# Kernel optimization log

Measured on AMD Instinct MI355X. Metric: run time of the kernel, lower is better.

## Reference

```python
import jax, jax.numpy as jnp
import numpy as np

M = 1024       # input feature dim
T_EXPERTS = 64 # number of experts
K = 2          # top-k
TOKENS = 65536 # B*N flattened tokens


def setup_inputs() -> dict:
    key = jax.random.key(0)
    ks = jax.random.split(key, 6)
    return {
        "x": jax.random.normal(ks[0], (TOKENS, M), dtype=jnp.float32),
        "noise": jax.random.normal(ks[1], (TOKENS, T_EXPERTS), dtype=jnp.float32),
        "Wg_w": jax.random.normal(ks[2], (T_EXPERTS, M), dtype=jnp.float32) * 0.02,
        "Wg_b": jax.random.normal(ks[3], (T_EXPERTS,), dtype=jnp.float32) * 0.02,
        "Wn_w": jax.random.normal(ks[4], (T_EXPERTS, M), dtype=jnp.float32) * 0.02,
        "Wn_b": jax.random.normal(ks[5], (T_EXPERTS,), dtype=jnp.float32) * 0.02,
    }


def reference(x, noise, Wg_w, Wg_b, Wn_w, Wn_b):
    # logits = Wg(x); noise_scale = softplus(Wnoise(x))
    logits = jnp.einsum("bm,tm->bt", x, Wg_w) + Wg_b          # [tokens, t]
    noise_scale = jax.nn.softplus(jnp.einsum("bm,tm->bt", x, Wn_w) + Wn_b)
    H = logits + noise * noise_scale                           # noisy logits
    topk_vals, topk_idx = jax.lax.top_k(H, K)                  # [tokens, k]
    topk_softmax = jax.nn.softmax(topk_vals, axis=-1)
    # scatter softmax weights into sparse [tokens, t] gate tensor
    rows = jnp.arange(H.shape[0])[:, None]
    gates = jnp.zeros_like(H).at[rows, topk_idx].set(topk_softmax)
    return (gates, H, topk_idx, noise_scale, logits)
```

## Files before the change

kernel.cpp:

```cpp
#include <hip/hip_runtime.h>
#include <math.h>

#define NTOK 65536
#define MDIM 1024
#define NE   64
#define TB   128
#define NKC  32
#define DELTA 5e-4f

typedef float f32x4  __attribute__((ext_vector_type(4)));
typedef float f32x2  __attribute__((ext_vector_type(2)));
typedef short bf16x8 __attribute__((ext_vector_type(8)));
typedef unsigned int u32;

__device__ __forceinline__ unsigned short f32_to_bf16_rne(float f) {
    u32 u = __builtin_bit_cast(u32, f);
    u32 r = u + 0x7FFFu + ((u >> 16) & 1u);
    return (unsigned short)(r >> 16);
}
__device__ __forceinline__ float bf16_to_f32(unsigned short h) {
    u32 u = ((u32)h) << 16;
    return __builtin_bit_cast(float, u);
}
__device__ __forceinline__ void gll16(const void* g, void* l) {
    __builtin_amdgcn_global_load_lds(
        (const __attribute__((address_space(1))) u32*)g,
        (__attribute__((address_space(3))) u32*)l, 16, 0, 0);
}
__device__ __forceinline__ void nt_store4(float* p, f32x4 v) {
    __builtin_nontemporal_store(v, (f32x4*)p);
}

__global__ __launch_bounds__(256) void split_w_kernel(
    const float* __restrict__ Wg_w, const float* __restrict__ Wn_w,
    unsigned short* __restrict__ ws, u32* __restrict__ cnt)
{
    if (blockIdx.x == 0 && threadIdx.x == 0) *cnt = 0;

    const int gid  = blockIdx.x * 256 + threadIdx.x;
    const int kc   = gid >> 10;
    const int rest = gid & 1023;
    const int tm   = rest >> 8;
    const int mat  = (rest >> 7) & 1;
    const int sp   = (rest >> 6) & 1;
    const int lane = rest & 63;
    const int e    = (lane & 15) + 16 * tm;
    const int k0   = kc * 32 + 8 * (lane >> 4);
    const float* W = mat ? Wn_w : Wg_w;

    unsigned short o[8];
#pragma unroll
    for (int i = 0; i < 8; ++i) {
        const float v = W[(size_t)e * MDIM + k0 + i];
        const u32 u  = __builtin_bit_cast(u32, v);
        const unsigned short hb = (unsigned short)(u >> 16);
        o[i] = sp ? f32_to_bf16_rne(v - bf16_to_f32(hb)) : hb;
    }
    uint4 pk;
    pk.x = (u32)o[0] | ((u32)o[1] << 16);
    pk.y = (u32)o[2] | ((u32)o[3] << 16);
    pk.z = (u32)o[4] | ((u32)o[5] << 16);
    pk.w = (u32)o[6] | ((u32)o[7] << 16);
    *reinterpret_cast<uint4*>(&ws[(size_t)gid * 8]) = pk;
}

__global__ __launch_bounds__(512, 4) void gate_mfma_kernel(
    const float* __restrict__ x,
    const float* __restrict__ noise,
    const unsigned short* __restrict__ ws,
    const float* __restrict__ Wg_b,
    const float* __restrict__ Wn_b,
    float* __restrict__ out_gates,
    float* __restrict__ out_H,
    float* __restrict__ out_idx,
    float* __restrict__ out_ns,
    float* __restrict__ out_logits,
    u32* __restrict__ cnt,
    u32* __restrict__ list)
{
    __shared__ unsigned short wbuf[2][8192];

    const int tid   = threadIdx.x;
    const int lane  = tid & 63;
    const int w     = tid >> 6;
    const int c     = lane & 15;
    const int q     = lane >> 4;
    const int tokw  = blockIdx.x * TB + w * 16;
    const int phase = blockIdx.x & (NKC - 1);

    const float* __restrict__ xr = x + (size_t)(tokw + c) * MDIM + 8 * q;

    f32x4 acc[4][2];
#pragma unroll
    for (int tm = 0; tm < 4; ++tm)
#pragma unroll
        for (int m = 0; m < 2; ++m)
            acc[tm][m] = (f32x4){0.f, 0.f, 0.f, 0.f};

    f32x4 xa, xb;

#define STAGE(CI, BUF)                                                          \
    {                                                                           \
        const unsigned short* wc_ = ws + (size_t)(CI) * 8192;                   \
        gll16(wc_ + (size_t)tid * 8,         &wbuf[BUF][(size_t)tid * 8]);      \
        gll16(wc_ + (size_t)(tid + 512) * 8, &wbuf[BUF][(size_t)(tid + 512) * 8]); \
        __builtin_amdgcn_sched_barrier(0);                                      \
        xa = *reinterpret_cast<const f32x4*>(xr + (CI) * 32);                   \
        xb = *reinterpret_cast<const f32x4*>(xr + (CI) * 32 + 4);               \
        __builtin_amdgcn_sched_barrier(0);                                      \
    }

    STAGE(phase, 0)
    asm volatile("s_waitcnt vmcnt(2)" ::: "memory");
    __syncthreads();

    int cur = 0;
    for (int kci = 0; kci < NKC; ++kci) {
        asm volatile("s_waitcnt vmcnt(0)" ::: "memory");

        bf16x8 xhi, xlo;
        {
            const float v[8] = {xa.x, xa.y, xa.z, xa.w, xb.x, xb.y, xb.z, xb.w};
            u32 hp[4], lp[4];
#pragma unroll
            for (int p = 0; p < 4; ++p) {
                const u32 u0 = __builtin_bit_cast(u32, v[2 * p]);
                const u32 u1 = __builtin_bit_cast(u32, v[2 * p + 1]);
                const float h0 = __builtin_bit_cast(float, u0 & 0xFFFF0000u);
                const float h1 = __builtin_bit_cast(float, u1 & 0xFFFF0000u);
                hp[p] = (u0 >> 16) | (u1 & 0xFFFF0000u);
                const u32 l0 = (u32)f32_to_bf16_rne(v[2 * p] - h0);
                const u32 l1 = (u32)f32_to_bf16_rne(v[2 * p + 1] - h1);
                lp[p] = l0 | (l1 << 16);
            }
            const uint4 h4 = {hp[0], hp[1], hp[2], hp[3]};
            const uint4 l4 = {lp[0], lp[1], lp[2], lp[3]};
            xhi = __builtin_bit_cast(bf16x8, h4);
            xlo = __builtin_bit_cast(bf16x8, l4);
        }

        if (kci + 1 < NKC) {
            const int kcn = (kci + 1 + phase) & (NKC - 1);
            STAGE(kcn, cur ^ 1)
        }

#pragma unroll
        for (int tm = 0; tm < 4; ++tm)
#pragma unroll
            for (int mat = 0; mat < 2; ++mat) {
                const int gbase = ((tm * 4 + mat * 2) * 64 + lane) * 8;
                const bf16x8 whi = *reinterpret_cast<const bf16x8*>(&wbuf[cur][gbase]);
                const bf16x8 wlo = *reinterpret_cast<const bf16x8*>(&wbuf[cur][gbase + 512]);
                f32x4 a = acc[tm][mat];
                a = __builtin_amdgcn_mfma_f32_16x16x32_bf16(wlo, xhi, a, 0, 0, 0);
                a = __builtin_amdgcn_mfma_f32_16x16x32_bf16(whi, xlo, a, 0, 0, 0);
                a = __builtin_amdgcn_mfma_f32_16x16x32_bf16(whi, xhi, a, 0, 0, 0);
                acc[tm][mat] = a;
            }

        if (kci + 1 < NKC) {
            asm volatile("s_waitcnt vmcnt(2)" ::: "memory");
            __syncthreads();
        }
        cur ^= 1;
    }
#undef STAGE

    f32x4 bgv[4], bnv[4];
#pragma unroll
    for (int tm = 0; tm < 4; ++tm) {
        bgv[tm] = *reinterpret_cast<const f32x4*>(&Wg_b[16 * tm + 4 * q]);
        bnv[tm] = *reinterpret_cast<const f32x4*>(&Wn_b[16 * tm + 4 * q]);
    }

    const int tok = tokw + c;
    float hv[4][4];

#pragma unroll
    for (int tm = 0; tm < 4; ++tm) {
        const size_t rb = (size_t)tok * NE + 16 * tm + 4 * q;
        const f32x4 nz = __builtin_nontemporal_load(
            reinterpret_cast<const f32x4*>(&noise[rb]));
        f32x4 lg, nsv, hh;
#pragma unroll
        for (int r = 0; r < 4; ++r) {
            lg[r] = acc[tm][0][r] + bgv[tm][r];
            const float nl = acc[tm][1][r] + bnv[tm][r];
            nsv[r] = fmaxf(nl, 0.f) + log1pf(expf(-fabsf(nl)));
            hh[r]  = fmaf(nz[r], nsv[r], lg[r]);
            hv[tm][r] = hh[r];
        }
        nt_store4(&out_logits[rb], lg);
        nt_store4(&out_ns[rb],     nsv);
        nt_store4(&out_H[rb],      hh);
    }

    float v1 = -INFINITY, v2 = -INFINITY, v3 = -INFINITY;
    int   i1 = 0,         i2 = 0;
#pragma unroll
    for (int tm = 0; tm < 4; ++tm)
#pragma unroll
        for (int r = 0; r < 4; ++r) {
            const int ex = 16 * tm + 4 * q + r;
            const float hcur = hv[tm][r];
            if (hcur > v1)      { v3 = v2; v2 = v1; i2 = i1; v1 = hcur; i1 = ex; }
            else if (hcur > v2) { v3 = v2; v2 = hcur; i2 = ex; }
            else if (hcur > v3) { v3 = hcur; }
        }

#pragma unroll
    for (int off = 16; off <= 32; off <<= 1) {
        const float w1 = __shfl_xor(v1, off, 64);
        const int   k1 = __shfl_xor(i1, off, 64);
        const float w2 = __shfl_xor(v2, off, 64);
        const int   k2 = __shfl_xor(i2, off, 64);
        const float w3 = __shfl_xor(v3, off, 64);
        float m3;
        if (v1 >= w1) m3 = (v2 >= w1) ? fmaxf(v3, w1) : fmaxf(v2, w2);
        else          m3 = (w2 >= v1) ? fmaxf(w3, v1) : fmaxf(w2, v2);
        if (w1 > v1 || (w1 == v1 && k1 < i1)) {
            if (v1 > w2 || (v1 == w2 && i1 < k2)) { v2 = v1; i2 = i1; }
            else                                  { v2 = w2; i2 = k2; }
            v1 = w1; i1 = k1;
        } else {
            if (w1 > v2 || (w1 == v2 && k1 < i2)) { v2 = w1; i2 = k1; }
        }
        v3 = m3;
    }

    const float e2v = expf(v2 - v1);
    const float inv = 1.f / (1.f + e2v);
    const float p1  = inv;
    const float p2  = e2v * inv;

#pragma unroll
    for (int tm = 0; tm < 4; ++tm) {
        f32x4 g;
#pragma unroll
        for (int r = 0; r < 4; ++r) {
            const int ex = 16 * tm + 4 * q + r;
            g[r] = (ex == i1) ? p1 : ((ex == i2) ? p2 : 0.f);
        }
        nt_store4(&out_gates[(size_t)tok * NE + 16 * tm + 4 * q], g);
    }
    if (q == 0) {
        f32x2 iv;
        iv.x = (float)i1;
        iv.y = (float)i2;
        __builtin_nontemporal_store(iv,
            reinterpret_cast<f32x2*>(&out_idx[(size_t)tok * 2]));
        if ((v1 - v2 < DELTA) || (v2 - v3 < DELTA)) {
            const u32 slot = atomicAdd(cnt, 1u);
            list[slot] = (u32)tok;
        }
    }
}

__global__ __launch_bounds__(64) void refine_kernel(
    const float* __restrict__ x,
    const float* __restrict__ noise,
    const float* __restrict__ Wg_w, const float* __restrict__ Wg_b,
    const float* __restrict__ Wn_w, const float* __restrict__ Wn_b,
    const u32* __restrict__ cnt, const u32* __restrict__ list,
    float* __restrict__ out_gates, float* __restrict__ out_idx)
{
    const int lane = threadIdx.x;
    const u32 n = *cnt;

    for (u32 it = blockIdx.x; it < n; it += gridDim.x) {
        const int tok = (int)list[it];

        f32x4 xv[4];
#pragma unroll
        for (int i = 0; i < 4; ++i)
            xv[i] = *reinterpret_cast<const f32x4*>(
                &x[(size_t)tok * MDIM + lane * 16 + i * 4]);

        float lgv = 0.f, nlv = 0.f;
        for (int e = 0; e < NE; ++e) {
            float sg = 0.f, sn = 0.f;
#pragma unroll
            for (int i = 0; i < 4; ++i) {
                const f32x4 wg = *reinterpret_cast<const f32x4*>(
                    &Wg_w[(size_t)e * MDIM + lane * 16 + i * 4]);
                const f32x4 wn = *reinterpret_cast<const f32x4*>(
                    &Wn_w[(size_t)e * MDIM + lane * 16 + i * 4]);
#pragma unroll
                for (int j = 0; j < 4; ++j) {
                    sg = fmaf(xv[i][j], wg[j], sg);
                    sn = fmaf(xv[i][j], wn[j], sn);
                }
            }
#pragma unroll
            for (int off = 32; off >= 1; off >>= 1) {
                sg += __shfl_xor(sg, off, 64);
                sn += __shfl_xor(sn, off, 64);
            }
            if (e == lane) { lgv = sg; nlv = sn; }
        }

        lgv += Wg_b[lane];
        nlv += Wn_b[lane];
        const float ns = fmaxf(nlv, 0.f) + log1pf(expf(-fabsf(nlv)));
        const float h  = fmaf(noise[(size_t)tok * NE + lane], ns, lgv);

        float v1 = h; int i1 = lane;
#pragma unroll
        for (int off = 32; off >= 1; off >>= 1) {
            const float ov = __shfl_xor(v1, off, 64);
            const int   oi = __shfl_xor(i1, off, 64);
            if (ov > v1 || (ov == v1 && oi < i1)) { v1 = ov; i1 = oi; }
        }
        float v2 = (lane == i1) ? -INFINITY : h; int i2 = lane;
#pragma unroll
        for (int off = 32; off >= 1; off >>= 1) {
            const float ov = __shfl_xor(v2, off, 64);
            const int   oi = __shfl_xor(i2, off, 64);
            if (ov > v2 || (ov == v2 && oi < i2)) { v2 = ov; i2 = oi; }
        }

        const float e2v = expf(v2 - v1);
        const float inv = 1.f / (1.f + e2v);
        const float p1  = inv;
        const float p2  = e2v * inv;

        out_gates[(size_t)tok * NE + lane] =
            (lane == i1) ? p1 : ((lane == i2) ? p2 : 0.f);
        if (lane == 0) {
            *reinterpret_cast<float2*>(&out_idx[(size_t)tok * 2]) =
                make_float2((float)i1, (float)i2);
        }
    }
}

extern "C" void kernel_launch(void* const* d_in, const int* in_sizes, int n_in,
                              void* d_out, int out_size, void* d_ws, size_t ws_size,
                              hipStream_t stream) {
    const float* x     = (const float*)d_in[0];
    const float* noise = (const float*)d_in[1];
    const float* Wg_w  = (const float*)d_in[2];
    const float* Wg_b  = (const float*)d_in[3];
    const float* Wn_w  = (const float*)d_in[4];
    const float* Wn_b  = (const float*)d_in[5];

    float* out = (float*)d_out;
    float* out_gates  = out;
    float* out_H      = out + (size_t)NTOK * NE;
    float* out_idx    = out + (size_t)2 * NTOK * NE;
    float* out_ns     = out + (size_t)2 * NTOK * NE + (size_t)NTOK * 2;
    float* out_logits = out + (size_t)3 * NTOK * NE + (size_t)NTOK * 2;

    unsigned short* wsplit = (unsigned short*)d_ws;
    u32* cnt  = (u32*)((char*)d_ws + 524288);
    u32* list = (u32*)((char*)d_ws + 524304);

    split_w_kernel<<<dim3(128), dim3(256), 0, stream>>>(Wg_w, Wn_w, wsplit, cnt);
    gate_mfma_kernel<<<dim3(NTOK / TB), dim3(512), 0, stream>>>(
        x, noise, wsplit, Wg_b, Wn_b,
        out_gates, out_H, out_idx, out_ns, out_logits, cnt, list);
    refine_kernel<<<dim3(1024), dim3(64), 0, stream>>>(
        x, noise, Wg_w, Wg_b, Wn_w, Wn_b, cnt, list, out_gates, out_idx);
}
```

Before: 123.9 us.

## Prefetch x two chunks ahead with double-buffered register bursts

Loads of x now arrive in bursts of two K-chunks, held in a double-buffered register set, and are issued about two iterations ahead instead of one. Weight staging into LDS stays one chunk ahead. The loop is fully unrolled and the vmcnt waits are adjusted so the compute never waits on the x burst that is still in flight. The goal is to hide global-memory latency for the streamed x reads, at the cost of more VGPRs, which may lower occupancy.

```diff
diff --git a/kernel.cpp b/kernel.cpp
--- a/kernel.cpp
+++ b/kernel.cpp
@@ -86,7 +86,7 @@
     const int c     = lane & 15;
     const int q     = lane >> 4;
     const int tokw  = blockIdx.x * TB + w * 16;
-    const int phase = blockIdx.x & (NKC - 1);
+    const int phase = (blockIdx.x & 15) * 2;
 
     const float* __restrict__ xr = x + (size_t)(tokw + c) * MDIM + 8 * q;
 
@@ -97,74 +97,100 @@
         for (int m = 0; m < 2; ++m)
             acc[tm][m] = (f32x4){0.f, 0.f, 0.f, 0.f};
 
-    f32x4 xa, xb;
-
-#define STAGE(CI, BUF)                                                          \
+    f32x4 xg[2][2][2];
+
+#define WGLL(CI, BUF)                                                           \
     {                                                                           \
         const unsigned short* wc_ = ws + (size_t)(CI) * 8192;                   \
         gll16(wc_ + (size_t)tid * 8,         &wbuf[BUF][(size_t)tid * 8]);      \
         gll16(wc_ + (size_t)(tid + 512) * 8, &wbuf[BUF][(size_t)(tid + 512) * 8]); \
         __builtin_amdgcn_sched_barrier(0);                                      \
-        xa = *reinterpret_cast<const f32x4*>(xr + (CI) * 32);                   \
-        xb = *reinterpret_cast<const f32x4*>(xr + (CI) * 32 + 4);               \
+    }
+#define XBURST(G, SET)                                                          \
+    {                                                                           \
+        const int c0_ = (phase + 2 * (G)) & (NKC - 1);                          \
+        const int c1_ = c0_ + 1;            \
+        xg[SET][0][0] = *reinterpret_cast<const f32x4*>(xr + c0_ * 32);         \
+        xg[SET][0][1] = *reinterpret_cast<const f32x4*>(xr + c0_ * 32 + 4);     \
+        xg[SET][1][0] = *reinterpret_cast<const f32x4*>(xr + c1_ * 32);         \
+        xg[SET][1][1] = *reinterpret_cast<const f32x4*>(xr + c1_ * 32 + 4);     \
         __builtin_amdgcn_sched_barrier(0);                                      \
     }
 
-    STAGE(phase, 0)
-    asm volatile("s_waitcnt vmcnt(2)" ::: "memory");
+    WGLL(phase, 0)
+    XBURST(0, 0)
+    XBURST(1, 1)
+    asm volatile("s_waitcnt vmcnt(8)" ::: "memory");
     __syncthreads();
 
     int cur = 0;
-    for (int kci = 0; kci < NKC; ++kci) {
-        asm volatile("s_waitcnt vmcnt(0)" ::: "memory");
-
-        bf16x8 xhi, xlo;
-        {
-            const float v[8] = {xa.x, xa.y, xa.z, xa.w, xb.x, xb.y, xb.z, xb.w};
-            u32 hp[4], lp[4];
-#pragma unroll
-            for (int p = 0; p < 4; ++p) {
-                const u32 u0 = __builtin_bit_cast(u32, v[2 * p]);
-                const u32 u1 = __builtin_bit_cast(u32, v[2 * p + 1]);
-                const float h0 = __builtin_bit_cast(float, u0 & 0xFFFF0000u);
-                const float h1 = __builtin_bit_cast(float, u1 & 0xFFFF0000u);
-                hp[p] = (u0 >> 16) | (u1 & 0xFFFF0000u);
-                const u32 l0 = (u32)f32_to_bf16_rne(v[2 * p] - h0);
-                const u32 l1 = (u32)f32_to_bf16_rne(v[2 * p + 1] - h1);
-                lp[p] = l0 | (l1 << 16);
-            }
-            const uint4 h4 = {hp[0], hp[1], hp[2], hp[3]};
-            const uint4 l4 = {lp[0], lp[1], lp[2], lp[3]};
-            xhi = __builtin_bit_cast(bf16x8, h4);
-            xlo = __builtin_bit_cast(bf16x8, l4);
-        }
-
-        if (kci + 1 < NKC) {
-            const int kcn = (kci + 1 + phase) & (NKC - 1);
-            STAGE(kcn, cur ^ 1)
-        }
-
-#pragma unroll
-        for (int tm = 0; tm < 4; ++tm)
-#pragma unroll
-            for (int mat = 0; mat < 2; ++mat) {
-                const int gbase = ((tm * 4 + mat * 2) * 64 + lane) * 8;
-                const bf16x8 whi = *reinterpret_cast<const bf16x8*>(&wbuf[cur][gbase]);
-                const bf16x8 wlo = *reinterpret_cast<const bf16x8*>(&wbuf[cur][gbase + 512]);
-                f32x4 a = acc[tm][mat];
-                a = __builtin_amdgcn_mfma_f32_16x16x32_bf16(wlo, xhi, a, 0, 0, 0);
-                a = __builtin_amdgcn_mfma_f32_16x16x32_bf16(whi, xlo, a, 0, 0, 0);
-                a = __builtin_amdgcn_mfma_f32_16x16x32_bf16(whi, xhi, a, 0, 0, 0);
-                acc[tm][mat] = a;
-            }
-
-        if (kci + 1 < NKC) {
-            asm volatile("s_waitcnt vmcnt(2)" ::: "memory");
-            __syncthreads();
-        }
-        cur ^= 1;
-    }
-#undef STAGE
+#pragma unroll
+    for (int g = 0; g < NKC / 2; ++g) {
+#pragma unroll
+        for (int j = 0; j < 2; ++j) {
+            const int i  = 2 * g + j;
+            const int st = g & 1;
+
+            bf16x8 xhi, xlo;
+            {
+                const f32x4 a = xg[st][j][0];
+                const f32x4 b = xg[st][j][1];
+                const float v[8] = {a.x, a.y, a.z, a.w, b.x, b.y, b.z, b.w};
+                u32 hp[4], lp[4];
+#pragma unroll
+                for (int p = 0; p < 4; ++p) {
+                    const u32 u0 = __builtin_bit_cast(u32, v[2 * p]);
+                    const u32 u1 = __builtin_bit_cast(u32, v[2 * p + 1]);
+                    const float h0 = __builtin_bit_cast(float, u0 & 0xFFFF0000u);
+                    const float h1 = __builtin_bit_cast(float, u1 & 0xFFFF0000u);
+                    hp[p] = (u0 >> 16) | (u1 & 0xFFFF0000u);
+                    const u32 l0 = (u32)f32_to_bf16_rne(v[2 * p] - h0);
+                    const u32 l1 = (u32)f32_to_bf16_rne(v[2 * p + 1] - h1);
+                    lp[p] = l0 | (l1 << 16);
+                }
+                const uint4 h4 = {hp[0], hp[1], hp[2], hp[3]};
+                const uint4 l4 = {lp[0], lp[1], lp[2], lp[3]};
+                xhi = __builtin_bit_cast(bf16x8, h4);
+                xlo = __builtin_bit_cast(bf16x8, l4);
+            }
+            __builtin_amdgcn_sched_barrier(0);
+
+            const bool have_next = (i + 1 < NKC);
+            if (have_next) {
+                WGLL((phase + i + 1) & (NKC - 1), cur ^ 1)
+            }
+            const bool do_burst = (j == 1) && (g + 2 < NKC / 2);
+            if (do_burst) {
+                XBURST(g + 2, st)
+            }
+
+#pragma unroll
+            for (int tm = 0; tm < 4; ++tm)
+#pragma unroll
+                for (int mat = 0; mat < 2; ++mat) {
+                    const int gbase = ((tm * 4 + mat * 2) * 64 + lane) * 8;
+                    const bf16x8 whi = *reinterpret_cast<const bf16x8*>(&wbuf[cur][gbase]);
+                    const bf16x8 wlo = *reinterpret_cast<const bf16x8*>(&wbuf[cur][gbase + 512]);
+                    f32x4 a = acc[tm][mat];
+                    a = __builtin_amdgcn_mfma_f32_16x16x32_bf16(wlo, xhi, a, 0, 0, 0);
+                    a = __builtin_amdgcn_mfma_f32_16x16x32_bf16(whi, xlo, a, 0, 0, 0);
+                    a = __builtin_amdgcn_mfma_f32_16x16x32_bf16(whi, xhi, a, 0, 0, 0);
+                    acc[tm][mat] = a;
+                }
+
+            if (have_next) {
+                if (do_burst) {
+                    asm volatile("s_waitcnt vmcnt(4)" ::: "memory");
+                } else {
+                    asm volatile("s_waitcnt vmcnt(0)" ::: "memory");
+                }
+                __syncthreads();
+                cur ^= 1;
+            }
+        }
+    }
+#undef WGLL
+#undef XBURST
 
     f32x4 bgv[4], bnv[4];
 #pragma unroll
```

After: 133.4 us. 7.7% more time.
